# Performance work log

Hardware: AMD Instinct MI355X
Metric: run time of the kernel (lower is better)

Reference implementation:

```python
import jax, jax.numpy as jnp
import numpy as np

B, T, E, H = 2, 4096, 768, 12
D = E // H  # head_dim = 64


def setup_inputs() -> dict:
    key = jax.random.key(0)
    ks = jax.random.split(key, 9)
    s = 1.0 / np.sqrt(E)
    return {
        "x": jax.random.normal(ks[0], (B, T, E), dtype=jnp.float32),
        "wq": jax.random.normal(ks[1], (E, E), dtype=jnp.float32) * s,
        "bq": jnp.zeros((E,), dtype=jnp.float32),
        "wk": jax.random.normal(ks[2], (E, E), dtype=jnp.float32) * s,
        "bk": jnp.zeros((E,), dtype=jnp.float32),
        "wv": jax.random.normal(ks[3], (E, E), dtype=jnp.float32) * s,
        "bv": jnp.zeros((E,), dtype=jnp.float32),
        "wo": jax.random.normal(ks[4], (E, E), dtype=jnp.float32) * s,
        "bo": jnp.zeros((E,), dtype=jnp.float32),
    }


def reference(x, wq, bq, wk, bk, wv, bv, wo, bo):
    # Linear projections (torch Linear: x @ W.T + b; weights here stored as (in,out))
    q = x @ wq + bq  # (B,T,E)
    k = x @ wk + bk
    v = x @ wv + bv

    def split(t):
        return t.reshape(B, T, H, D).transpose(0, 2, 1, 3)  # (B,H,T,D)

    q, k, v = split(q), split(k), split(v)
    scale = 1.0 / np.sqrt(D).astype(np.float32)
    scores = jnp.einsum("bhtd,bhsd->bhts", q, k) * scale  # (B,H,T,T)
    causal = jnp.tril(jnp.ones((T, T), dtype=bool))
    scores = jnp.where(causal, scores, -jnp.inf)
    attn = jax.nn.softmax(scores, axis=-1)
    out = jnp.einsum("bhts,bhsd->bhtd", attn, v)  # (B,H,T,D)
    out = out.transpose(0, 2, 1, 3).reshape(B, T, E)
    return out @ wo + bo
```

## Files before the change

### kernel.cpp

```cpp
#include <hip/hip_runtime.h>
#include <hip/hip_bf16.h>

#define TSEQ 4096
#define EMB 768
#define NH 12
#define DH 64
#define BT 8192

typedef __attribute__((ext_vector_type(8))) short bf16x8;
typedef __attribute__((ext_vector_type(4))) float f32x4;

#define FENCE() asm volatile("" ::: "memory")

__device__ __forceinline__ f32x4 mfma16(bf16x8 a, bf16x8 b, f32x4 c) {
    return __builtin_amdgcn_mfma_f32_16x16x32_bf16(a, b, c, 0, 0, 0);
}

__device__ __forceinline__ void gload16(const void* g, void* l) {
    __builtin_amdgcn_global_load_lds((const __attribute__((address_space(1))) void*)g,
                                     (__attribute__((address_space(3))) void*)l, 16, 0, 0);
}

__global__ __launch_bounds__(256) void conv_x_k(const float* __restrict__ x,
                                                __hip_bfloat16* __restrict__ xb) {
    int i = (blockIdx.x * 256 + threadIdx.x) * 4;
    float4 v = *(const float4*)(x + i);
    union { unsigned short u[4]; uint2 p; } o;
    __hip_bfloat16 t0 = __float2bfloat16(v.x); o.u[0] = *(unsigned short*)&t0;
    __hip_bfloat16 t1 = __float2bfloat16(v.y); o.u[1] = *(unsigned short*)&t1;
    __hip_bfloat16 t2 = __float2bfloat16(v.z); o.u[2] = *(unsigned short*)&t2;
    __hip_bfloat16 t3 = __float2bfloat16(v.w); o.u[3] = *(unsigned short*)&t3;
    *(uint2*)(xb + i) = o.p;
}

__global__ __launch_bounds__(256) void conv_w_k(const float* w0, const float* w1,
                                                const float* w2, const float* w3,
                                                __hip_bfloat16* o0, __hip_bfloat16* o1,
                                                __hip_bfloat16* o2, __hip_bfloat16* o3) {
    const float* w; __hip_bfloat16* o;
    switch (blockIdx.z) {
        case 0: w = w0; o = o0; break;
        case 1: w = w1; o = o1; break;
        case 2: w = w2; o = o2; break;
        default: w = w3; o = o3; break;
    }
    __shared__ float tile[32][33];
    int tx = threadIdx.x & 31, ty = threadIdx.x >> 5;
    int kb = blockIdx.y * 32, nb = blockIdx.x * 32;
    for (int i = 0; i < 32; i += 8)
        tile[ty + i][tx] = w[(size_t)(kb + ty + i) * EMB + nb + tx];
    __syncthreads();
    for (int i = 0; i < 32; i += 8)
        o[(size_t)(nb + ty + i) * EMB + kb + tx] = __float2bfloat16(tile[tx][ty + i]);
}

__device__ __forceinline__ void gemm_body(const __hip_bfloat16* __restrict__ A,
                                          const __hip_bfloat16* __restrict__ Wt,
                                          const float* __restrict__ bias,
                                          void* __restrict__ outp, int mode, float scale) {
    __shared__ alignas(16) char As[2][8192];
    __shared__ alignas(16) char Bs[2][8192];
    const int m0 = blockIdx.x * 128, n0 = blockIdx.y * 128;
    const int tid = threadIdx.x;
    const int lane = tid & 63, l15 = lane & 15, lg = lane >> 4;
    const int wave = tid >> 6, wm = wave >> 1, wn = wave & 1;
    const int swz = (l15 & 7) << 4;

    int mrow_[2]; int kelem_[2];
#pragma unroll
    for (int c = 0; c < 2; ++c) {
        int p = c * 4096 + tid * 16;
        int lrow = p >> 7, w = p & 127;
        int wp = w ^ ((lrow & 7) << 4);
        mrow_[c] = lrow + ((wp >> 6) & 1) * 64;
        kelem_[c] = (wp & 63) >> 1;
    }

    f32x4 acc[4][4];
    for (int i = 0; i < 4; ++i)
        for (int j = 0; j < 4; ++j) acc[i][j] = (f32x4){0.f, 0.f, 0.f, 0.f};

    auto stage = [&](int buf, int k0) {
#pragma unroll
        for (int c = 0; c < 2; ++c)
            gload16(A + (size_t)(m0 + mrow_[c]) * EMB + k0 + kelem_[c],
                    As[buf] + c * 4096 + wave * 1024);
#pragma unroll
        for (int c = 0; c < 2; ++c)
            gload16(Wt + (size_t)(n0 + mrow_[c]) * EMB + k0 + kelem_[c],
                    Bs[buf] + c * 4096 + wave * 1024);
    };

    stage(0, 0);
    const int NK = EMB / 32;
    for (int ks = 0; ks < NK; ++ks) {
        const int cur = ks & 1;
        const bool pre = (ks + 1 < NK);
        if (pre) stage(cur ^ 1, (ks + 1) * 32);
        if (pre) asm volatile("s_waitcnt vmcnt(4)" ::: "memory");
        else     asm volatile("s_waitcnt vmcnt(0)" ::: "memory");
        FENCE(); __builtin_amdgcn_s_barrier(); FENCE();
        bf16x8 af[4], bfv[4];
#pragma unroll
        for (int f = 0; f < 4; ++f)
            af[f] = *(const bf16x8*)(As[cur] + (f * 16 + l15) * 128 + ((wm * 64 + lg * 16) ^ swz));
#pragma unroll
        for (int f = 0; f < 4; ++f)
            bfv[f] = *(const bf16x8*)(Bs[cur] + (f * 16 + l15) * 128 + ((wn * 64 + lg * 16) ^ swz));
        __builtin_amdgcn_s_setprio(1);
#pragma unroll
        for (int i = 0; i < 4; ++i)
#pragma unroll
            for (int j = 0; j < 4; ++j)
                acc[i][j] = mfma16(af[i], bfv[j], acc[i][j]);
        __builtin_amdgcn_s_setprio(0);
        FENCE(); __builtin_amdgcn_s_barrier(); FENCE();
    }

#pragma unroll
    for (int i = 0; i < 4; ++i) {
#pragma unroll
        for (int j = 0; j < 4; ++j) {
            const int n = n0 + wn * 64 + j * 16 + l15;
            const float bv = bias[n];
            const int mbase = m0 + wm * 64 + i * 16 + lg * 4;
#pragma unroll
            for (int r = 0; r < 4; ++r) {
                const int m = mbase + r;
                const float val = (acc[i][j][r] + bv) * scale;
                if (mode == 2) {
                    ((float*)outp)[(size_t)m * EMB + n] = val;
                } else {
                    const int b = m >> 12, t = m & (TSEQ - 1);
                    const int h = n >> 6, d = n & 63;
                    size_t addr;
                    if (mode == 0) addr = ((size_t)(b * NH + h) * TSEQ + t) * DH + d;
                    else           addr = ((size_t)(b * NH + h) * DH + d) * TSEQ + t;
                    ((__hip_bfloat16*)outp)[addr] = __float2bfloat16(val);
                }
            }
        }
    }
}

__global__ __launch_bounds__(256) void qkv_k(const __hip_bfloat16* __restrict__ xb,
                                             const __hip_bfloat16* __restrict__ wqT,
                                             const __hip_bfloat16* __restrict__ wkT,
                                             const __hip_bfloat16* __restrict__ wvT,
                                             const float* __restrict__ bq,
                                             const float* __restrict__ bk,
                                             const float* __restrict__ bv,
                                             __hip_bfloat16* __restrict__ qo,
                                             __hip_bfloat16* __restrict__ ko,
                                             __hip_bfloat16* __restrict__ vo) {
    const __hip_bfloat16* Wt; const float* bias; void* o; int mode; float scale;
    const float cq = 0.125f * 1.44269504089f;
    switch (blockIdx.z) {
        case 0:  Wt = wqT; bias = bq; o = qo; mode = 0; scale = cq;  break;
        case 1:  Wt = wkT; bias = bk; o = ko; mode = 0; scale = 1.f; break;
        default: Wt = wvT; bias = bv; o = vo; mode = 1; scale = 1.f; break;
    }
    gemm_body(xb, Wt, bias, o, mode, scale);
}

__global__ __launch_bounds__(256) void oproj64_k(const __hip_bfloat16* __restrict__ A,
                                                 const __hip_bfloat16* __restrict__ Wt,
                                                 const float* __restrict__ bias,
                                                 float* __restrict__ out) {
    __shared__ alignas(16) char As[2][4096];
    __shared__ alignas(16) char Bs[2][8192];
    const int m0 = blockIdx.x * 64, n0 = blockIdx.y * 128;
    const int tid = threadIdx.x;
    const int lane = tid & 63, l15 = lane & 15, lg = lane >> 4;
    const int wave = tid >> 6, wm = wave >> 1, wn = wave & 1;
    const int swz = (l15 & 7) << 4;

    int amrow, akelem;
    {
        int p = tid * 16;
        int lrow = p >> 7, w = p & 127;
        int wp = w ^ ((lrow & 7) << 4);
        amrow = lrow + ((wp >> 6) & 1) * 32;
        akelem = (wp & 63) >> 1;
    }
    int bnrow[2], bkelem[2];
#pragma unroll
    for (int c = 0; c < 2; ++c) {
        int p = c * 4096 + tid * 16;
        int lrow = p >> 7, w = p & 127;
        int wp = w ^ ((lrow & 7) << 4);
        bnrow[c] = lrow + ((wp >> 6) & 1) * 64;
        bkelem[c] = (wp & 63) >> 1;
    }

    f32x4 acc[2][4];
    for (int i = 0; i < 2; ++i)
        for (int j = 0; j < 4; ++j) acc[i][j] = (f32x4){0.f, 0.f, 0.f, 0.f};

    auto stage = [&](int buf, int k0) {
        gload16(A + (size_t)(m0 + amrow) * EMB + k0 + akelem,
                As[buf] + wave * 1024);
#pragma unroll
        for (int c = 0; c < 2; ++c)
            gload16(Wt + (size_t)(n0 + bnrow[c]) * EMB + k0 + bkelem[c],
                    Bs[buf] + c * 4096 + wave * 1024);
    };

    stage(0, 0);
    const int NK = EMB / 32;
    for (int ks = 0; ks < NK; ++ks) {
        const int cur = ks & 1;
        const bool pre = (ks + 1 < NK);
        if (pre) stage(cur ^ 1, (ks + 1) * 32);
        if (pre) asm volatile("s_waitcnt vmcnt(3)" ::: "memory");
        else     asm volatile("s_waitcnt vmcnt(0)" ::: "memory");
        FENCE(); __builtin_amdgcn_s_barrier(); FENCE();
        bf16x8 af[2], bfv[4];
#pragma unroll
        for (int f = 0; f < 2; ++f)
            af[f] = *(const bf16x8*)(As[cur] + (f * 16 + l15) * 128 + ((wm * 64 + lg * 16) ^ swz));
#pragma unroll
        for (int f = 0; f < 4; ++f)
            bfv[f] = *(const bf16x8*)(Bs[cur] + (f * 16 + l15) * 128 + ((wn * 64 + lg * 16) ^ swz));
        __builtin_amdgcn_s_setprio(1);
#pragma unroll
        for (int i = 0; i < 2; ++i)
#pragma unroll
            for (int j = 0; j < 4; ++j)
                acc[i][j] = mfma16(af[i], bfv[j], acc[i][j]);
        __builtin_amdgcn_s_setprio(0);
        FENCE(); __builtin_amdgcn_s_barrier(); FENCE();
    }

#pragma unroll
    for (int i = 0; i < 2; ++i) {
#pragma unroll
        for (int j = 0; j < 4; ++j) {
            const int n = n0 + wn * 64 + j * 16 + l15;
            const float bv = bias[n];
            const int mbase = m0 + wm * 32 + i * 16 + lg * 4;
#pragma unroll
            for (int r = 0; r < 4; ++r)
                out[(size_t)(mbase + r) * EMB + n] = acc[i][j][r] + bv;
        }
    }
}

__global__ __launch_bounds__(256, 3) void attn_k(const __hip_bfloat16* __restrict__ qb,
                                                 const __hip_bfloat16* __restrict__ kb,
                                                 const __hip_bfloat16* __restrict__ vt,
                                                 __hip_bfloat16* __restrict__ ab) {
    __shared__ alignas(16) char Ks[2][8192];
    __shared__ alignas(16) char Vs[2][8192];
    __shared__ alignas(16) char pbuf[4][4096];
    const int lane = threadIdx.x & 63, l15 = lane & 15, lg = lane >> 4;
    const int wave = threadIdx.x >> 6;
    const int bid = blockIdx.x;
    const int xcd = bid & 7, slot = bid >> 3;
    const int hgrp = slot >> 5;
    const int pair = ((slot & 31) + hgrp * 11) & 31;
    const int bh = xcd + hgrp * 8;
    const __hip_bfloat16* Qh = qb + (size_t)bh * TSEQ * DH;
    const __hip_bfloat16* Kh = kb + (size_t)bh * TSEQ * DH;
    const __hip_bfloat16* Vh = vt + (size_t)bh * DH * TSEQ;
    char* Pb = pbuf[wave];
    const int swz = (l15 & 7) << 4;
    const int b = bh / NH, h = bh % NH;
    const float M0 = 12.0f;

    bf16x8 ones8;
#pragma unroll
    for (int j = 0; j < 8; ++j) ones8[j] = (short)0x3F80;

    unsigned ka[8];
#pragma unroll
    for (int st = 0; st < 4; ++st)
#pragma unroll
        for (int ks = 0; ks < 2; ++ks)
            ka[st * 2 + ks] = (unsigned)((st * 16 + l15) * 128 + ((ks * 64 + lg * 16) ^ swz));
    char* pwh[4]; char* prh[2]; char* pwl[4]; char* prl[2];
#pragma unroll
    for (int st = 0; st < 4; ++st) {
        pwh[st] = Pb + l15 * 128 + ((st * 32 + lg * 8) ^ swz);
        pwl[st] = pwh[st] + 2048;
    }
#pragma unroll
    for (int ks = 0; ks < 2; ++ks) {
        prh[ks] = Pb + l15 * 128 + ((ks * 64 + lg * 16) ^ swz);
        prl[ks] = prh[ks] + 2048;
    }
    const int dthr = wave * 16 + l15 - lg * 4;

    int r_[2], wp_[2];
#pragma unroll
    for (int c = 0; c < 2; ++c) {
        int p = c * 4096 + wave * 1024 + lane * 16;
        int r = p >> 7, w = p & 127;
        r_[c] = r;
        wp_[c] = (w ^ ((r & 7) << 4)) >> 1;
    }

    const int lo = pair, hi = 63 - pair;
    const int q0l = lo * 64 + wave * 16;
    const int q0h = hi * 64 + wave * 16;
    const int nsb = hi + 1;

    bf16x8 qh0 = *(const bf16x8*)(Qh + (size_t)(q0h + l15) * DH + lg * 8);
    bf16x8 qh1 = *(const bf16x8*)(Qh + (size_t)(q0h + l15) * DH + 32 + lg * 8);
    bf16x8 ql0 = *(const bf16x8*)(Qh + (size_t)(q0l + l15) * DH + lg * 8);
    bf16x8 ql1 = *(const bf16x8*)(Qh + (size_t)(q0l + l15) * DH + 32 + lg * 8);

    f32x4 oh[4], ol[4];
#pragma unroll
    for (int dt = 0; dt < 4; ++dt) { oh[dt] = (f32x4){0.f,0.f,0.f,0.f}; ol[dt] = (f32x4){0.f,0.f,0.f,0.f}; }
    f32x4 lh = (f32x4){0.f,0.f,0.f,0.f}, ll = (f32x4){0.f,0.f,0.f,0.f};

    const char* kg0 = (const char*)(Kh + (size_t)r_[0] * DH + wp_[0]);
    const char* kg1 = (const char*)(Kh + (size_t)r_[1] * DH + wp_[1]);
    const char* vg0 = (const char*)(Vh + (size_t)r_[0] * TSEQ + wp_[0]);
    const char* vg1 = (const char*)(Vh + (size_t)r_[1] * TSEQ + wp_[1]);

#define STAGE(DST) do {                                                          \
    gload16(kg0, Ks[DST] + wave * 1024);                                         \
    gload16(kg1, Ks[DST] + 4096 + wave * 1024);                                  \
    gload16(vg0, Vs[DST] + wave * 1024);                                         \
    gload16(vg1, Vs[DST] + 4096 + wave * 1024);                                  \
    kg0 += 8192; kg1 += 8192; vg0 += 128; vg1 += 128;                            \
} while (0)

#define QKSM(KF, Q0, Q1, MASKB, PW) do {                                         \
    f32x4 sa[4];                                                                 \
    __builtin_amdgcn_s_setprio(1);                                               \
    _Pragma("unroll")                                                            \
    for (int st = 0; st < 4; ++st) {                                             \
        f32x4 z = (f32x4){0.f, 0.f, 0.f, 0.f};                                   \
        z = mfma16(KF[st * 2 + 0], Q0, z);                                       \
        z = mfma16(KF[st * 2 + 1], Q1, z);                                       \
        sa[st] = z;                                                              \
    }                                                                            \
    __builtin_amdgcn_s_setprio(0);                                               \
    if (MASKB) {                                                                 \
        _Pragma("unroll")                                                        \
        for (int st = 0; st < 4; ++st)                                           \
            _Pragma("unroll")                                                    \
            for (int r = 0; r < 4; ++r)                                          \
                if (st * 16 + r > dthr) sa[st][r] = -INFINITY;                   \
    }                                                                            \
    _Pragma("unroll")                                                            \
    for (int st = 0; st < 4; ++st) {                                             \
        const float e0 = exp2f(sa[st][0] - M0);                                  \
        const float e1 = exp2f(sa[st][1] - M0);                                  \
        const float e2 = exp2f(sa[st][2] - M0);                                  \
        const float e3 = exp2f(sa[st][3] - M0);                                  \
        uint2 pkv;                                                               \
        asm("v_cvt_pk_bf16_f32 %0, %1, %2" : "=v"(pkv.x) : "v"(e0), "v"(e1));    \
        asm("v_cvt_pk_bf16_f32 %0, %1, %2" : "=v"(pkv.y) : "v"(e2), "v"(e3));    \
        *(uint2*)PW[st] = pkv;                                                   \
    }                                                                            \
} while (0)

#define PVU(VF, OV, LA, PR) do {                                                 \
    bf16x8 pf0 = *(const bf16x8*)PR[0];                                          \
    bf16x8 pf1 = *(const bf16x8*)PR[1];                                          \
    __builtin_amdgcn_s_setprio(1);                                               \
    LA = mfma16(pf0, ones8, LA);                                                 \
    LA = mfma16(pf1, ones8, LA);                                                 \
    _Pragma("unroll")                                                            \
    for (int dt = 0; dt < 4; ++dt)                                               \
        OV[dt] = mfma16(pf0, VF[dt * 2 + 0], OV[dt]);                            \
    _Pragma("unroll")                                                            \
    for (int dt = 0; dt < 4; ++dt)                                               \
        OV[dt] = mfma16(pf1, VF[dt * 2 + 1], OV[dt]);                            \
    __builtin_amdgcn_s_setprio(0);                                               \
} while (0)

#define SBODY(BUF, PRE, LOACT, MHI, MLO) do {                                    \
    asm volatile("s_waitcnt vmcnt(0)" ::: "memory");                             \
    FENCE(); __builtin_amdgcn_s_barrier(); FENCE();                              \
    if (PRE) STAGE((BUF) ^ 1);                                                   \
    bf16x8 kf[8];                                                                \
    _Pragma("unroll")                                                            \
    for (int i = 0; i < 8; ++i) kf[i] = *(const bf16x8*)(Ks[BUF] + ka[i]);       \
    QKSM(kf, qh0, qh1, MHI, pwh);                                                \
    if (LOACT) QKSM(kf, ql0, ql1, MLO, pwl);                                     \
    bf16x8 vf[8];                                                                \
    _Pragma("unroll")                                                            \
    for (int i = 0; i < 8; ++i) vf[i] = *(const bf16x8*)(Vs[BUF] + ka[i]);       \
    asm volatile("s_waitcnt lgkmcnt(0)" ::: "memory");                           \
    PVU(vf, oh, lh, prh);                                                        \
    if (LOACT) PVU(vf, ol, ll, prl);                                             \
} while (0)

    STAGE(0);
    int sb = 0;
    while (sb + 2 <= nsb) {
        SBODY(0, true, sb <= lo, false, sb == lo);
        SBODY(1, sb + 2 < nsb, sb + 1 <= lo, sb + 1 == nsb - 1, sb + 1 == lo);
        sb += 2;
    }
    if (sb < nsb) SBODY(0, false, sb <= lo, true, sb == lo);

#undef SBODY
#undef PVU
#undef QKSM
#undef STAGE

    {
        float inv[4];
#pragma unroll
        for (int r = 0; r < 4; ++r) inv[r] = 1.0f / lh[r];
#pragma unroll
        for (int r = 0; r < 4; ++r) {
            const int qrow = q0h + lg * 4 + r;
            const size_t rowbase = ((size_t)b * TSEQ + qrow) * EMB + h * DH;
#pragma unroll
            for (int dt = 0; dt < 4; ++dt)
                ab[rowbase + dt * 16 + l15] = __float2bfloat16(oh[dt][r] * inv[r]);
        }
    }
    {
        float inv[4];
#pragma unroll
        for (int r = 0; r < 4; ++r) inv[r] = 1.0f / ll[r];
#pragma unroll
        for (int r = 0; r < 4; ++r) {
            const int qrow = q0l + lg * 4 + r;
            const size_t rowbase = ((size_t)b * TSEQ + qrow) * EMB + h * DH;
#pragma unroll
            for (int dt = 0; dt < 4; ++dt)
                ab[rowbase + dt * 16 + l15] = __float2bfloat16(ol[dt][r] * inv[r]);
        }
    }
}

extern "C" void kernel_launch(void* const* d_in, const int* in_sizes, int n_in,
                              void* d_out, int out_size, void* d_ws, size_t ws_size,
                              hipStream_t stream) {
    (void)in_sizes; (void)n_in; (void)out_size; (void)ws_size;
    const float* x  = (const float*)d_in[0];
    const float* wq = (const float*)d_in[1];
    const float* bq = (const float*)d_in[2];
    const float* wk = (const float*)d_in[3];
    const float* bk = (const float*)d_in[4];
    const float* wv = (const float*)d_in[5];
    const float* bv = (const float*)d_in[6];
    const float* wo = (const float*)d_in[7];
    const float* bo = (const float*)d_in[8];
    float* out = (float*)d_out;

    char* ws = (char*)d_ws;
    size_t off = 0;
    auto alloc = [&](size_t bytes) {
        char* p = ws + off;
        off += (bytes + 255) & ~(size_t)255;
        return p;
    };
    __hip_bfloat16* xb  = (__hip_bfloat16*)alloc((size_t)BT * EMB * 2);
    __hip_bfloat16* qbf = (__hip_bfloat16*)alloc((size_t)BT * EMB * 2);
    __hip_bfloat16* kbf = (__hip_bfloat16*)alloc((size_t)BT * EMB * 2);
    __hip_bfloat16* vtb = (__hip_bfloat16*)alloc((size_t)BT * EMB * 2);
    __hip_bfloat16* abf = (__hip_bfloat16*)alloc((size_t)BT * EMB * 2);
    __hip_bfloat16* wqT = (__hip_bfloat16*)alloc((size_t)EMB * EMB * 2);
    __hip_bfloat16* wkT = (__hip_bfloat16*)alloc((size_t)EMB * EMB * 2);
    __hip_bfloat16* wvT = (__hip_bfloat16*)alloc((size_t)EMB * EMB * 2);
    __hip_bfloat16* woT = (__hip_bfloat16*)alloc((size_t)EMB * EMB * 2);

    conv_x_k<<<BT * EMB / 1024, 256, 0, stream>>>(x, xb);
    conv_w_k<<<dim3(24, 24, 4), 256, 0, stream>>>(wq, wk, wv, wo, wqT, wkT, wvT, woT);
    qkv_k<<<dim3(64, 6, 3), 256, 0, stream>>>(xb, wqT, wkT, wvT, bq, bk, bv, qbf, kbf, vtb);
    attn_k<<<768, 256, 0, stream>>>(qbf, kbf, vtb, abf);
    oproj64_k<<<dim3(128, 6), 256, 0, stream>>>(abf, woT, bo, out);
}
```

Measured before the change: 189.7 us.

## Merge conversion kernels, use single-barrier GEMM loop, simplify attention block mapping

Folds the x conversion and the weight transpose/convert into one launch so a kernel launch is dropped. Both GEMM main loops now wait on all loads and do one barrier before issuing the next prefetch, instead of prefetching first and using two barriers. This saves a barrier per step, but each tile's load is no longer overlapped with the wait. The attention block-to-pair mapping also drops its rotation by head group, which changes the load balance of causal tiles across XCDs.

```diff
diff --git a/kernel.cpp b/kernel.cpp
--- a/kernel.cpp
+++ b/kernel.cpp
@@ -21,32 +21,36 @@
                                      (__attribute__((address_space(3))) void*)l, 16, 0, 0);
 }
 
-__global__ __launch_bounds__(256) void conv_x_k(const float* __restrict__ x,
-                                                __hip_bfloat16* __restrict__ xb) {
-    int i = (blockIdx.x * 256 + threadIdx.x) * 4;
-    float4 v = *(const float4*)(x + i);
-    union { unsigned short u[4]; uint2 p; } o;
-    __hip_bfloat16 t0 = __float2bfloat16(v.x); o.u[0] = *(unsigned short*)&t0;
-    __hip_bfloat16 t1 = __float2bfloat16(v.y); o.u[1] = *(unsigned short*)&t1;
-    __hip_bfloat16 t2 = __float2bfloat16(v.z); o.u[2] = *(unsigned short*)&t2;
-    __hip_bfloat16 t3 = __float2bfloat16(v.w); o.u[3] = *(unsigned short*)&t3;
-    *(uint2*)(xb + i) = o.p;
-}
-
-__global__ __launch_bounds__(256) void conv_w_k(const float* w0, const float* w1,
-                                                const float* w2, const float* w3,
-                                                __hip_bfloat16* o0, __hip_bfloat16* o1,
-                                                __hip_bfloat16* o2, __hip_bfloat16* o3) {
+__global__ __launch_bounds__(256) void conv_all_k(const float* __restrict__ x,
+                                                  __hip_bfloat16* __restrict__ xb,
+                                                  const float* w0, const float* w1,
+                                                  const float* w2, const float* w3,
+                                                  __hip_bfloat16* o0, __hip_bfloat16* o1,
+                                                  __hip_bfloat16* o2, __hip_bfloat16* o3) {
+    __shared__ float tile[32][33];
+    int bid = blockIdx.x;
+    if (bid < 6144) {
+        int i = (bid * 256 + threadIdx.x) * 4;
+        float4 v = *(const float4*)(x + i);
+        union { unsigned short u[4]; uint2 p; } o;
+        __hip_bfloat16 t0 = __float2bfloat16(v.x); o.u[0] = *(unsigned short*)&t0;
+        __hip_bfloat16 t1 = __float2bfloat16(v.y); o.u[1] = *(unsigned short*)&t1;
+        __hip_bfloat16 t2 = __float2bfloat16(v.z); o.u[2] = *(unsigned short*)&t2;
+        __hip_bfloat16 t3 = __float2bfloat16(v.w); o.u[3] = *(unsigned short*)&t3;
+        *(uint2*)(xb + i) = o.p;
+        return;
+    }
+    bid -= 6144;
+    const int z = bid / 576, rr = bid % 576, by = rr / 24, bx = rr % 24;
     const float* w; __hip_bfloat16* o;
-    switch (blockIdx.z) {
+    switch (z) {
         case 0: w = w0; o = o0; break;
         case 1: w = w1; o = o1; break;
         case 2: w = w2; o = o2; break;
         default: w = w3; o = o3; break;
     }
-    __shared__ float tile[32][33];
     int tx = threadIdx.x & 31, ty = threadIdx.x >> 5;
-    int kb = blockIdx.y * 32, nb = blockIdx.x * 32;
+    int kb = by * 32, nb = bx * 32;
     for (int i = 0; i < 32; i += 8)
         tile[ty + i][tx] = w[(size_t)(kb + ty + i) * EMB + nb + tx];
     __syncthreads();
@@ -95,11 +99,9 @@
     const int NK = EMB / 32;
     for (int ks = 0; ks < NK; ++ks) {
         const int cur = ks & 1;
-        const bool pre = (ks + 1 < NK);
-        if (pre) stage(cur ^ 1, (ks + 1) * 32);
-        if (pre) asm volatile("s_waitcnt vmcnt(4)" ::: "memory");
-        else     asm volatile("s_waitcnt vmcnt(0)" ::: "memory");
+        asm volatile("s_waitcnt vmcnt(0)" ::: "memory");
         FENCE(); __builtin_amdgcn_s_barrier(); FENCE();
+        if (ks + 1 < NK) stage(cur ^ 1, (ks + 1) * 32);
         bf16x8 af[4], bfv[4];
 #pragma unroll
         for (int f = 0; f < 4; ++f)
@@ -114,7 +116,6 @@
             for (int j = 0; j < 4; ++j)
                 acc[i][j] = mfma16(af[i], bfv[j], acc[i][j]);
         __builtin_amdgcn_s_setprio(0);
-        FENCE(); __builtin_amdgcn_s_barrier(); FENCE();
     }
 
 #pragma unroll
@@ -210,11 +211,9 @@
     const int NK = EMB / 32;
     for (int ks = 0; ks < NK; ++ks) {
         const int cur = ks & 1;
-        const bool pre = (ks + 1 < NK);
-        if (pre) stage(cur ^ 1, (ks + 1) * 32);
-        if (pre) asm volatile("s_waitcnt vmcnt(3)" ::: "memory");
-        else     asm volatile("s_waitcnt vmcnt(0)" ::: "memory");
+        asm volatile("s_waitcnt vmcnt(0)" ::: "memory");
         FENCE(); __builtin_amdgcn_s_barrier(); FENCE();
+        if (ks + 1 < NK) stage(cur ^ 1, (ks + 1) * 32);
         bf16x8 af[2], bfv[4];
 #pragma unroll
         for (int f = 0; f < 2; ++f)
@@ -229,7 +228,6 @@
             for (int j = 0; j < 4; ++j)
                 acc[i][j] = mfma16(af[i], bfv[j], acc[i][j]);
         __builtin_amdgcn_s_setprio(0);
-        FENCE(); __builtin_amdgcn_s_barrier(); FENCE();
     }
 
 #pragma unroll
@@ -257,8 +255,7 @@
     const int wave = threadIdx.x >> 6;
     const int bid = blockIdx.x;
     const int xcd = bid & 7, slot = bid >> 3;
-    const int hgrp = slot >> 5;
-    const int pair = ((slot & 31) + hgrp * 11) & 31;
+    const int pair = slot & 31, hgrp = slot >> 5;
     const int bh = xcd + hgrp * 8;
     const __hip_bfloat16* Qh = qb + (size_t)bh * TSEQ * DH;
     const __hip_bfloat16* Kh = kb + (size_t)bh * TSEQ * DH;
@@ -465,8 +462,7 @@
     __hip_bfloat16* wvT = (__hip_bfloat16*)alloc((size_t)EMB * EMB * 2);
     __hip_bfloat16* woT = (__hip_bfloat16*)alloc((size_t)EMB * EMB * 2);
 
-    conv_x_k<<<BT * EMB / 1024, 256, 0, stream>>>(x, xb);
-    conv_w_k<<<dim3(24, 24, 4), 256, 0, stream>>>(wq, wk, wv, wo, wqT, wkT, wvT, woT);
+    conv_all_k<<<6144 + 2304, 256, 0, stream>>>(x, xb, wq, wk, wv, wo, wqT, wkT, wvT, woT);
     qkv_k<<<dim3(64, 6, 3), 256, 0, stream>>>(xb, wqT, wkT, wvT, bq, bk, bv, qbf, kbf, vtb);
     attn_k<<<768, 256, 0, stream>>>(qbf, kbf, vtb, abf);
     oproj64_k<<<dim3(128, 6), 256, 0, stream>>>(abf, woT, bo, out);
```

After: 186.0 us. Within noise of the previous version (-1.9%).
